# Kernel optimization log

Measured on AMD Instinct MI355X. Metric: run time of the kernel, lower is better.

Reference implementation:

```python
import jax, jax.numpy as jnp
import numpy as np
import math

NUM_BUCKETS = 32
MAX_DISTANCE = 128
NUM_HEADS = 16
D_MODEL = 1024
HEAD_DIM = D_MODEL // NUM_HEADS


def _relative_position_bucket(relative_position, num_buckets=NUM_BUCKETS, max_distance=MAX_DISTANCE):
    # bidirectional=False path of the original
    rp = -jnp.minimum(relative_position, 0)  # non-negative distances
    max_exact = num_buckets // 2
    is_small = rp < max_exact
    rp_safe = jnp.maximum(rp, 1).astype(jnp.float32)
    rp_if_large = max_exact + (
        jnp.log(rp_safe / max_exact) / math.log(max_distance / max_exact) * (num_buckets - max_exact)
    ).astype(jnp.int32)
    rp_if_large = jnp.minimum(rp_if_large, num_buckets - 1)
    return jnp.where(is_small, rp, rp_if_large)


def relative_bias(rab_weight, q_len, k_len):
    ctx = jnp.arange(q_len)[:, None]
    mem = jnp.arange(k_len)[None, :]
    buckets = _relative_position_bucket(mem - ctx)  # [Q, K]
    vals = rab_weight[buckets]                       # [Q, K, H]
    return jnp.transpose(vals, (2, 0, 1))[None]      # [1, H, Q, K]


def setup_inputs() -> dict:
    key = jax.random.key(0)
    k1, k2, k3, k4 = jax.random.split(key, 4)
    B, S = 4, 2048
    return {
        "v": jax.random.normal(k1, (B, S, D_MODEL), dtype=jnp.float32),
        "k": jax.random.normal(k2, (B, S, D_MODEL), dtype=jnp.float32),
        "q": jax.random.normal(k3, (B, S, D_MODEL), dtype=jnp.float32),
        "rab_weight": jax.random.normal(k4, (NUM_BUCKETS, NUM_HEADS), dtype=jnp.float32),
    }


def reference(v, k, q, rab_weight):
    B, S, _ = q.shape
    def split(x):
        return jnp.transpose(x.reshape(B, S, NUM_HEADS, HEAD_DIM), (0, 2, 1, 3))  # [B,H,S,D]
    qh, kh, vh = split(q), split(k), split(v)
    scores = jnp.einsum("bhqd,bhkd->bhqk", qh, kh)          # [B,H,S,S]
    scores = scores + relative_bias(rab_weight, S, S)        # add relative bias
    av = jnp.einsum("bhqk,bhkd->bhqd", jax.nn.silu(scores), vh)
    return jnp.transpose(av, (0, 2, 1, 3)).reshape(B, S, D_MODEL)
```

## Files before the change

kernel.cpp:

```cpp
#include <hip/hip_runtime.h>

#define NB 4
#define SEQ 2048
#define NH 16
#define HD 64
#define DMODEL 1024

typedef short bf16x8 __attribute__((ext_vector_type(8)));
typedef float f32x16 __attribute__((ext_vector_type(16)));

union FragU {
    bf16x8 v;
    uint2 u2[2];
    unsigned short s[8];
};

__device__ __forceinline__ unsigned int f2bf_bits(float x) {
    unsigned int u = __float_as_uint(x);
    return (u + 0x8000u) >> 16;
}

__device__ __forceinline__ float silu_f(float s) {
    float e = __builtin_amdgcn_exp2f(s * -1.44269504f);
    return s * __builtin_amdgcn_rcpf(1.0f + e);
}

__global__ __launch_bounds__(256, 2)
void paa_kernel(const float* __restrict__ Vg, const float* __restrict__ Kg,
                const float* __restrict__ Qg, const float* __restrict__ RW,
                float* __restrict__ Og)
{
    __shared__ __align__(16) unsigned short KsLds[64 * 68];
    __shared__ __align__(16) unsigned short VtLds[64 * 68];
    __shared__ float btab[128];

    const int tid  = threadIdx.x;
    const int lane = tid & 63;
    const int wave = tid >> 6;
    const int half = lane >> 5;
    const int l31  = lane & 31;

    const int bid  = blockIdx.x;
    const int bh   = bid & 63;
    const int qt   = bid >> 6;
    const int b    = bh >> 4;
    const int head = bh & 15;

    const int q0w = qt * 256 + wave * 64;

    if (tid < 128) {
        int rp = tid;
        int bucket;
        if (rp < 16) bucket = rp;
        else {
            int big = 16 + (int)(logf((float)rp * 0.0625f) * 7.6943736f);
            bucket = big < 31 ? big : 31;
        }
        btab[tid] = RW[bucket * NH + head];
    }

    FragU qf[2][4];
    {
        const float* qbase = Qg + (size_t)(b * SEQ) * DMODEL + head * HD;
        #pragma unroll
        for (int u = 0; u < 2; ++u) {
            const float* qrow = qbase + (size_t)(q0w + u * 32 + l31) * DMODEL;
            #pragma unroll
            for (int kf = 0; kf < 4; ++kf) {
                int dd = kf * 16 + half * 8;
                float4 x0 = *(const float4*)(qrow + dd);
                float4 x1 = *(const float4*)(qrow + dd + 4);
                FragU f;
                f.s[0] = f2bf_bits(x0.x); f.s[1] = f2bf_bits(x0.y);
                f.s[2] = f2bf_bits(x0.z); f.s[3] = f2bf_bits(x0.w);
                f.s[4] = f2bf_bits(x1.x); f.s[5] = f2bf_bits(x1.y);
                f.s[6] = f2bf_bits(x1.z); f.s[7] = f2bf_bits(x1.w);
                qf[u][kf] = f;
            }
        }
    }

    f32x16 oacc[2][2];
    #pragma unroll
    for (int u = 0; u < 2; ++u)
        #pragma unroll
        for (int n = 0; n < 2; ++n)
            #pragma unroll
            for (int r = 0; r < 16; ++r) oacc[u][n][r] = 0.0f;

    __syncthreads();
    const float bias_d0  = btab[0];
    const float bias_far = btab[127];

    const float* kbase = Kg + (size_t)(b * SEQ) * DMODEL + head * HD;
    const float* vbase = Vg + (size_t)(b * SEQ) * DMODEL + head * HD;
    const int kc4 = tid >> 4;
    const int d4  = tid & 15;

    for (int it = 0; it < 32; ++it) {
        const int kcb = it * 64;

        #pragma unroll
        for (int i = 0; i < 4; ++i) {
            int f = tid + i * 256;
            int row = f >> 4;
            int c4  = f & 15;
            float4 x = *(const float4*)(kbase + (size_t)(kcb + row) * DMODEL + c4 * 4);
            uint2 w;
            w.x = f2bf_bits(x.x) | (f2bf_bits(x.y) << 16);
            w.y = f2bf_bits(x.z) | (f2bf_bits(x.w) << 16);
            *(uint2*)&KsLds[row * 68 + c4 * 4] = w;
        }
        {
            float a[4][4];
            #pragma unroll
            for (int r = 0; r < 4; ++r) {
                float4 x = *(const float4*)(vbase + (size_t)(kcb + kc4 * 4 + r) * DMODEL + d4 * 4);
                a[r][0] = x.x; a[r][1] = x.y; a[r][2] = x.z; a[r][3] = x.w;
            }
            #pragma unroll
            for (int c = 0; c < 4; ++c) {
                uint2 w;
                w.x = f2bf_bits(a[0][c]) | (f2bf_bits(a[1][c]) << 16);
                w.y = f2bf_bits(a[2][c]) | (f2bf_bits(a[3][c]) << 16);
                *(uint2*)&VtLds[(d4 * 4 + c) * 68 + kc4 * 4] = w;
            }
        }
        __syncthreads();

        f32x16 st[2][2];
        #pragma unroll
        for (int t = 0; t < 2; ++t)
            #pragma unroll
            for (int u = 0; u < 2; ++u)
                #pragma unroll
                for (int r = 0; r < 16; ++r) st[t][u][r] = 0.0f;

        #pragma unroll
        for (int t = 0; t < 2; ++t) {
            #pragma unroll
            for (int kf = 0; kf < 4; ++kf) {
                FragU ka;
                int off = (t * 32 + l31) * 68 + kf * 16 + half * 8;
                ka.u2[0] = *(const uint2*)&KsLds[off];
                ka.u2[1] = *(const uint2*)&KsLds[off + 4];
                #pragma unroll
                for (int u = 0; u < 2; ++u)
                    st[t][u] = __builtin_amdgcn_mfma_f32_32x32x16_bf16(
                        ka.v, qf[u][kf].v, st[t][u], 0, 0, 0);
            }
        }

        FragU pf[2][4];
        #pragma unroll
        for (int t = 0; t < 2; ++t) {
            const int kcmin = kcb + t * 32;
            #pragma unroll
            for (int u = 0; u < 2; ++u) {
                const int qminu = q0w + u * 32;
                float vals[16];
                if (qminu + 31 - kcmin <= 0) {
                    #pragma unroll
                    for (int r = 0; r < 16; ++r) vals[r] = silu_f(st[t][u][r] + bias_d0);
                } else if (qminu - (kcmin + 31) >= 113) {
                    #pragma unroll
                    for (int r = 0; r < 16; ++r) vals[r] = silu_f(st[t][u][r] + bias_far);
                } else {
                    const int dql = qminu + l31 - kcmin - 4 * half;
                    #pragma unroll
                    for (int r = 0; r < 16; ++r) {
                        int dv = dql - ((r & 3) + 8 * (r >> 2));
                        dv = dv < 0 ? 0 : (dv > 127 ? 127 : dv);
                        vals[r] = silu_f(st[t][u][r] + btab[dv]);
                    }
                }
                #pragma unroll
                for (int r = 0; r < 8; ++r) pf[u][t * 2].s[r]     = f2bf_bits(vals[r]);
                #pragma unroll
                for (int r = 0; r < 8; ++r) pf[u][t * 2 + 1].s[r] = f2bf_bits(vals[r + 8]);
            }
        }

        #pragma unroll
        for (int f = 0; f < 4; ++f) {
            #pragma unroll
            for (int n = 0; n < 2; ++n) {
                FragU vf;
                int off = (n * 32 + l31) * 68 + f * 16 + half * 4;
                vf.u2[0] = *(const uint2*)&VtLds[off];
                vf.u2[1] = *(const uint2*)&VtLds[off + 8];
                #pragma unroll
                for (int u = 0; u < 2; ++u)
                    oacc[u][n] = __builtin_amdgcn_mfma_f32_32x32x16_bf16(
                        pf[u][f].v, vf.v, oacc[u][n], 0, 0, 0);
            }
        }
        __syncthreads();
    }

    float* obase = Og + (size_t)(b * SEQ) * DMODEL + head * HD;
    #pragma unroll
    for (int u = 0; u < 2; ++u) {
        #pragma unroll
        for (int r = 0; r < 16; ++r) {
            int q = q0w + u * 32 + (r & 3) + 8 * (r >> 2) + 4 * half;
            float* orow = obase + (size_t)q * DMODEL;
            #pragma unroll
            for (int n = 0; n < 2; ++n)
                orow[n * 32 + l31] = oacc[u][n][r];
        }
    }
}

extern "C" void kernel_launch(void* const* d_in, const int* in_sizes, int n_in,
                              void* d_out, int out_size, void* d_ws, size_t ws_size,
                              hipStream_t stream) {
    const float* v  = (const float*)d_in[0];
    const float* k  = (const float*)d_in[1];
    const float* q  = (const float*)d_in[2];
    const float* rw = (const float*)d_in[3];
    float* out = (float*)d_out;
    paa_kernel<<<dim3(512), dim3(256), 0, stream>>>(v, k, q, rw, out);
}
```

Measured before the change: 227.3 us.

## Prefetch next K/V tile into registers, fold bias and exp scale into MFMA

Loads the next K and V tile into registers while the current tile is being computed, so global-load latency overlaps with MFMA work. Initializes the score accumulators with the relative bias instead of adding it afterwards. Pre-scales Q and the bias by log2(e) so silu needs no multiply before exp2, then rescales the output by ln2. Replaces the per-element bf16 rounding with packed conversions. These add register pressure and slightly change rounding, because Q is scaled before the bf16 conversion.

```diff
diff --git a/kernel.cpp b/kernel.cpp
--- a/kernel.cpp
+++ b/kernel.cpp
@@ -12,18 +12,27 @@
 union FragU {
     bf16x8 v;
     uint2 u2[2];
+    unsigned int w[4];
     unsigned short s[8];
 };
 
-__device__ __forceinline__ unsigned int f2bf_bits(float x) {
-    unsigned int u = __float_as_uint(x);
-    return (u + 0x8000u) >> 16;
-}
-
-__device__ __forceinline__ float silu_f(float s) {
-    float e = __builtin_amdgcn_exp2f(s * -1.44269504f);
-    return s * __builtin_amdgcn_rcpf(1.0f + e);
-}
+#if __has_builtin(__builtin_amdgcn_cvt_pk_bf16_f32)
+typedef __bf16 v2bf_t __attribute__((ext_vector_type(2)));
+__device__ __forceinline__ unsigned int pack_bf16(float lo, float hi) {
+    union { v2bf_t h; unsigned int u; } cv;
+    cv.h = __builtin_amdgcn_cvt_pk_bf16_f32(lo, hi);
+    return cv.u;
+}
+#else
+__device__ __forceinline__ unsigned int pack_bf16(float lo, float hi) {
+    unsigned int a = __float_as_uint(lo) + 0x8000u;
+    unsigned int b = __float_as_uint(hi) + 0x8000u;
+    return __builtin_amdgcn_perm(b, a, 0x07060302);
+}
+#endif
+
+#define EXP_SCALE 1.44269504f
+#define LN2       0.69314718f
 
 __global__ __launch_bounds__(256, 2)
 void paa_kernel(const float* __restrict__ Vg, const float* __restrict__ Kg,
@@ -56,7 +65,7 @@
             int big = 16 + (int)(logf((float)rp * 0.0625f) * 7.6943736f);
             bucket = big < 31 ? big : 31;
         }
-        btab[tid] = RW[bucket * NH + head];
+        btab[tid] = RW[bucket * NH + head] * EXP_SCALE;
     }
 
     FragU qf[2][4];
@@ -71,10 +80,10 @@
                 float4 x0 = *(const float4*)(qrow + dd);
                 float4 x1 = *(const float4*)(qrow + dd + 4);
                 FragU f;
-                f.s[0] = f2bf_bits(x0.x); f.s[1] = f2bf_bits(x0.y);
-                f.s[2] = f2bf_bits(x0.z); f.s[3] = f2bf_bits(x0.w);
-                f.s[4] = f2bf_bits(x1.x); f.s[5] = f2bf_bits(x1.y);
-                f.s[6] = f2bf_bits(x1.z); f.s[7] = f2bf_bits(x1.w);
+                f.w[0] = pack_bf16(x0.x * EXP_SCALE, x0.y * EXP_SCALE);
+                f.w[1] = pack_bf16(x0.z * EXP_SCALE, x0.w * EXP_SCALE);
+                f.w[2] = pack_bf16(x1.x * EXP_SCALE, x1.y * EXP_SCALE);
+                f.w[3] = pack_bf16(x1.z * EXP_SCALE, x1.w * EXP_SCALE);
                 qf[u][kf] = f;
             }
         }
@@ -92,92 +101,106 @@
     const float bias_d0  = btab[0];
     const float bias_far = btab[127];
 
-    const float* kbase = Kg + (size_t)(b * SEQ) * DMODEL + head * HD;
-    const float* vbase = Vg + (size_t)(b * SEQ) * DMODEL + head * HD;
-    const int kc4 = tid >> 4;
-    const int d4  = tid & 15;
+    const int krow0 = tid >> 4;
+    const int c4    = tid & 15;
+    const int kc4   = tid >> 4;
+    const int d4    = tid & 15;
+
+    const float* kthr = Kg + (size_t)(b * SEQ) * DMODEL + head * HD
+                      + (size_t)krow0 * DMODEL + c4 * 4;
+    const float* vthr = Vg + (size_t)(b * SEQ) * DMODEL + head * HD
+                      + (size_t)(kc4 * 4) * DMODEL + d4 * 4;
+
+    float4 kreg[4], vreg[4];
+    #pragma unroll
+    for (int i = 0; i < 4; ++i) kreg[i] = *(const float4*)(kthr + (size_t)(i * 16) * DMODEL);
+    #pragma unroll
+    for (int r = 0; r < 4; ++r) vreg[r] = *(const float4*)(vthr + (size_t)r * DMODEL);
 
     for (int it = 0; it < 32; ++it) {
         const int kcb = it * 64;
 
         #pragma unroll
         for (int i = 0; i < 4; ++i) {
-            int f = tid + i * 256;
-            int row = f >> 4;
-            int c4  = f & 15;
-            float4 x = *(const float4*)(kbase + (size_t)(kcb + row) * DMODEL + c4 * 4);
             uint2 w;
-            w.x = f2bf_bits(x.x) | (f2bf_bits(x.y) << 16);
-            w.y = f2bf_bits(x.z) | (f2bf_bits(x.w) << 16);
-            *(uint2*)&KsLds[row * 68 + c4 * 4] = w;
+            w.x = pack_bf16(kreg[i].x, kreg[i].y);
+            w.y = pack_bf16(kreg[i].z, kreg[i].w);
+            *(uint2*)&KsLds[(krow0 + i * 16) * 68 + c4 * 4] = w;
         }
         {
-            float a[4][4];
-            #pragma unroll
-            for (int r = 0; r < 4; ++r) {
-                float4 x = *(const float4*)(vbase + (size_t)(kcb + kc4 * 4 + r) * DMODEL + d4 * 4);
-                a[r][0] = x.x; a[r][1] = x.y; a[r][2] = x.z; a[r][3] = x.w;
-            }
+            const float* vr = (const float*)vreg;
             #pragma unroll
             for (int c = 0; c < 4; ++c) {
                 uint2 w;
-                w.x = f2bf_bits(a[0][c]) | (f2bf_bits(a[1][c]) << 16);
-                w.y = f2bf_bits(a[2][c]) | (f2bf_bits(a[3][c]) << 16);
+                w.x = pack_bf16(vr[0 * 4 + c], vr[1 * 4 + c]);
+                w.y = pack_bf16(vr[2 * 4 + c], vr[3 * 4 + c]);
                 *(uint2*)&VtLds[(d4 * 4 + c) * 68 + kc4 * 4] = w;
             }
         }
         __syncthreads();
 
-        f32x16 st[2][2];
-        #pragma unroll
-        for (int t = 0; t < 2; ++t)
-            #pragma unroll
-            for (int u = 0; u < 2; ++u)
-                #pragma unroll
-                for (int r = 0; r < 16; ++r) st[t][u][r] = 0.0f;
-
-        #pragma unroll
-        for (int t = 0; t < 2; ++t) {
-            #pragma unroll
-            for (int kf = 0; kf < 4; ++kf) {
-                FragU ka;
-                int off = (t * 32 + l31) * 68 + kf * 16 + half * 8;
-                ka.u2[0] = *(const uint2*)&KsLds[off];
-                ka.u2[1] = *(const uint2*)&KsLds[off + 4];
-                #pragma unroll
-                for (int u = 0; u < 2; ++u)
-                    st[t][u] = __builtin_amdgcn_mfma_f32_32x32x16_bf16(
-                        ka.v, qf[u][kf].v, st[t][u], 0, 0, 0);
-            }
+        if (it < 31) {
+            const float* kn = kthr + (size_t)(kcb + 64) * DMODEL;
+            const float* vn = vthr + (size_t)(kcb + 64) * DMODEL;
+            #pragma unroll
+            for (int i = 0; i < 4; ++i) kreg[i] = *(const float4*)(kn + (size_t)(i * 16) * DMODEL);
+            #pragma unroll
+            for (int r = 0; r < 4; ++r) vreg[r] = *(const float4*)(vn + (size_t)r * DMODEL);
         }
 
         FragU pf[2][4];
         #pragma unroll
         for (int t = 0; t < 2; ++t) {
             const int kcmin = kcb + t * 32;
+            FragU ka[4];
+            #pragma unroll
+            for (int kf = 0; kf < 4; ++kf) {
+                int off = (t * 32 + l31) * 68 + kf * 16 + half * 8;
+                ka[kf].u2[0] = *(const uint2*)&KsLds[off];
+                ka[kf].u2[1] = *(const uint2*)&KsLds[off + 4];
+            }
+            f32x16 st[2];
             #pragma unroll
             for (int u = 0; u < 2; ++u) {
                 const int qminu = q0w + u * 32;
-                float vals[16];
                 if (qminu + 31 - kcmin <= 0) {
                     #pragma unroll
-                    for (int r = 0; r < 16; ++r) vals[r] = silu_f(st[t][u][r] + bias_d0);
+                    for (int r = 0; r < 16; ++r) st[u][r] = bias_d0;
                 } else if (qminu - (kcmin + 31) >= 113) {
                     #pragma unroll
-                    for (int r = 0; r < 16; ++r) vals[r] = silu_f(st[t][u][r] + bias_far);
+                    for (int r = 0; r < 16; ++r) st[u][r] = bias_far;
                 } else {
                     const int dql = qminu + l31 - kcmin - 4 * half;
                     #pragma unroll
                     for (int r = 0; r < 16; ++r) {
                         int dv = dql - ((r & 3) + 8 * (r >> 2));
                         dv = dv < 0 ? 0 : (dv > 127 ? 127 : dv);
-                        vals[r] = silu_f(st[t][u][r] + btab[dv]);
+                        st[u][r] = btab[dv];
                     }
                 }
-                #pragma unroll
-                for (int r = 0; r < 8; ++r) pf[u][t * 2].s[r]     = f2bf_bits(vals[r]);
-                #pragma unroll
-                for (int r = 0; r < 8; ++r) pf[u][t * 2 + 1].s[r] = f2bf_bits(vals[r + 8]);
+            }
+            #pragma unroll
+            for (int kf = 0; kf < 4; ++kf)
+                #pragma unroll
+                for (int u = 0; u < 2; ++u)
+                    st[u] = __builtin_amdgcn_mfma_f32_32x32x16_bf16(
+                        ka[kf].v, qf[u][kf].v, st[u], 0, 0, 0);
+
+            #pragma unroll
+            for (int u = 0; u < 2; ++u) {
+                float vals[16];
+                #pragma unroll
+                for (int r = 0; r < 16; ++r) {
+                    float x = st[u][r];
+                    float e = __builtin_amdgcn_exp2f(-x);
+                    vals[r] = x * __builtin_amdgcn_rcpf(1.0f + e);
+                }
+                #pragma unroll
+                for (int j = 0; j < 4; ++j)
+                    pf[u][t * 2].w[j]     = pack_bf16(vals[2 * j], vals[2 * j + 1]);
+                #pragma unroll
+                for (int j = 0; j < 4; ++j)
+                    pf[u][t * 2 + 1].w[j] = pack_bf16(vals[8 + 2 * j], vals[9 + 2 * j]);
             }
         }
 
@@ -207,7 +230,7 @@
             float* orow = obase + (size_t)q * DMODEL;
             #pragma unroll
             for (int n = 0; n < 2; ++n)
-                orow[n * 32 + l31] = oacc[u][n][r];
+                orow[n * 32 + l31] = oacc[u][n][r] * LN2;
         }
     }
 }
```

Result: slower. 252.5 us (+11.1%).
